# Performance work log

Measured on AMD Instinct MI355X. Metric: run time of the kernel, lower is better.

## Reference

```python
import jax, jax.numpy as jnp
import numpy as np


def gcn_conv(x, W, b, src, dst, num_nodes):
    # PyG GCNConv: h = D^{-1/2} (A + I) D^{-1/2} (x W) + b
    h = x @ W  # [N, H]
    ones = jnp.ones(src.shape[0], dtype=h.dtype)
    deg = jax.ops.segment_sum(ones, dst, num_segments=num_nodes) + 1.0  # +1 for self-loop
    d_inv_sqrt = jax.lax.rsqrt(deg)
    norm = d_inv_sqrt[src] * d_inv_sqrt[dst]  # [E]
    msg = h[src] * norm[:, None]  # [E, H] gather
    agg = jax.ops.segment_sum(msg, dst, num_segments=num_nodes)  # scatter-add
    agg = agg + h * (1.0 / deg)[:, None]  # self-loop term: deg_i^{-1/2} * deg_i^{-1/2}
    return agg + b


def setup_inputs() -> dict:
    key = jax.random.key(0)
    ks = jax.random.split(key, 10)
    N, E, F, H, C, G = 100000, 1000000, 64, 128, 2, 512
    x = jax.random.normal(ks[0], (N, F), dtype=jnp.float32)
    edge_index = jax.random.randint(ks[1], (2, E), 0, N, dtype=jnp.int64)
    batch = jnp.sort(jax.random.randint(ks[2], (N,), 0, G, dtype=jnp.int64))
    s1 = 1.0 / np.sqrt(F)
    s2 = 1.0 / np.sqrt(H)
    W1 = jax.random.normal(ks[3], (F, H), dtype=jnp.float32) * s1
    b1 = jnp.zeros((H,), dtype=jnp.float32)
    W2 = jax.random.normal(ks[4], (H, H), dtype=jnp.float32) * s2
    b2 = jnp.zeros((H,), dtype=jnp.float32)
    Wfc = jax.random.normal(ks[5], (H, C), dtype=jnp.float32) * s2
    bfc = jnp.zeros((C,), dtype=jnp.float32)
    return {"x": x, "edge_index": edge_index, "batch": batch, "num_graphs": G,
            "W1": W1, "b1": b1, "W2": W2, "b2": b2, "Wfc": Wfc, "bfc": bfc}


def reference(x, edge_index, batch, num_graphs, W1, b1, W2, b2, Wfc, bfc):
    # Dropout is inference-mode (identity), matching model.eval().
    N = x.shape[0]
    src, dst = edge_index[0], edge_index[1]
    h = gcn_conv(x, W1, b1, src, dst, N)
    h = jax.nn.relu(h)
    h = gcn_conv(h, W2, b2, src, dst, N)
    h = jax.nn.relu(h)
    # global mean pool over graphs
    summed = jax.ops.segment_sum(h, batch, num_segments=num_graphs)  # [G, H]
    counts = jax.ops.segment_sum(jnp.ones((N,), h.dtype), batch, num_segments=num_graphs)
    pooled = summed / jnp.maximum(counts, 1.0)[:, None]
    logits = pooled @ Wfc + bfc  # [G, C]
    return jax.nn.softmax(logits, axis=1)
```

## Files before the change

### kernel.cpp

```cpp
#include <hip/hip_runtime.h>
#include <hip/hip_bf16.h>

typedef __hip_bfloat16 bf16;
typedef __attribute__((ext_vector_type(8))) short short8;
typedef __attribute__((ext_vector_type(4))) float f32x4;
typedef __attribute__((ext_vector_type(2))) float f32x2;

#define FDIM 64
#define HDIM 128

#define ESTRIDE 4096
#define EC 8192
#define ECPT (EC / 256)

__device__ __forceinline__ float b2f(bf16 v) { return __bfloat162float(v); }
__device__ __forceinline__ float bits2f(unsigned int u) {
    return __uint_as_float(u << 16);
}
__device__ __forceinline__ unsigned short f2bits(float f) {
    bf16 b = __float2bfloat16(f);
    return *reinterpret_cast<unsigned short*>(&b);
}
__device__ __forceinline__ unsigned char f2fp8(float v) {
    int pk = __builtin_amdgcn_cvt_pk_fp8_f32(v, v, 0, false);
    return (unsigned char)(pk & 0xFF);
}

__device__ __forceinline__ int edge_word(const int* e, long long logical_idx, int is64) {
    return is64 ? e[2 * logical_idx] : e[logical_idx];
}

__global__ __launch_bounds__(256) void k_phase1(const int* __restrict__ edge,
                                                int* __restrict__ gcur,
                                                int* __restrict__ ebuf,
                                                int E,
                                                const void* __restrict__ W1, const void* __restrict__ b1,
                                                const void* __restrict__ W2, const void* __restrict__ b2,
                                                const void* __restrict__ Wfc, const void* __restrict__ bfc,
                                                bf16* __restrict__ W1t, bf16* __restrict__ W2t,
                                                bf16* __restrict__ b1c, bf16* __restrict__ b2c,
                                                bf16* __restrict__ Wfcc, bf16* __restrict__ bfcc,
                                                const void* __restrict__ x,
                                                unsigned char* __restrict__ X8,
                                                int totalX4,
                                                int* __restrict__ flags,
                                                const int* __restrict__ batch,
                                                int* __restrict__ gstart,
                                                int N, int G,
                                                int NB1, int WB, int XB) {
    int blk = blockIdx.x;
    int tid = threadIdx.x;
    if (blk < NB1) {
        unsigned long long zb = __ballot(edge[2 * (tid & 63) + 1] == 0);
        int is64 = (__popcll(zb) > 32);
        __shared__ int h[512];
        for (int b2 = tid; b2 < 512; b2 += 256) h[b2] = 0;
        __syncthreads();
        int e0 = blk * EC;
        int dcache[ECPT];
#pragma unroll
        for (int k = 0; k < ECPT; k++) {
            int i = e0 + (k << 8) + tid;
            int d = -1;
            if (i < E) d = edge_word(edge, (long long)E + i, is64);
            dcache[k] = d;
            if (d >= 0) atomicAdd(&h[(d >> 8) & 511], 1);
        }
        __syncthreads();
        for (int b2 = tid; b2 < 512; b2 += 256) {
            int c = h[b2];
            h[b2] = c ? atomicAdd(&gcur[b2], c) : 0;
        }
        __syncthreads();
#pragma unroll
        for (int k = 0; k < ECPT; k++) {
            int i = e0 + (k << 8) + tid;
            int d = dcache[k];
            if (d >= 0) {
                int s = edge_word(edge, i, is64);
                int bb = (d >> 8) & 511;
                int pos = atomicAdd(&h[bb], 1);
                if ((unsigned)pos < (unsigned)ESTRIDE)
                    ebuf[(bb << 12) + pos] = s | ((d & 255) << 24);
            }
        }
    } else if (blk < NB1 + WB) {
        const unsigned short* w1u = (const unsigned short*)W1;
        unsigned short wv = w1u[2 * (tid & 63)];
        int ee = (wv >> 7) & 0xFF;
        unsigned long long wb2 = __ballot(ee == 0 || ee >= 137);
        int f0 = (__popcll(wb2) > 4);
        if (blk == NB1 && tid == 0) flags[0] = f0;
        int gid = (blk - NB1) * 256 + tid;
        int stride = WB * 256;
#define CV(src, si) (f0 ? __float2bfloat16(((const float*)(src))[si]) : ((const bf16*)(src))[si])
        for (int i = gid; i < FDIM * HDIM; i += stride) {
            int n = i >> 6, k = i & 63;
            W1t[i] = CV(W1, k * HDIM + n);
        }
        for (int i = gid; i < HDIM * HDIM; i += stride) {
            int n = i >> 7, k = i & 127;
            W2t[i] = CV(W2, k * HDIM + n);
        }
        for (int i = gid; i < HDIM; i += stride) b1c[i] = CV(b1, i);
        for (int i = gid; i < HDIM; i += stride) b2c[i] = CV(b2, i);
        for (int i = gid; i < HDIM * 2; i += stride) Wfcc[i] = CV(Wfc, i);
        for (int i = gid; i < 2; i += stride) bfcc[i] = CV(bfc, i);
#undef CV
    } else if (blk < NB1 + WB + XB) {
        const unsigned short* w1u = (const unsigned short*)W1;
        unsigned short wv = w1u[2 * (tid & 63)];
        int ee = (wv >> 7) & 0xFF;
        unsigned long long wb2 = __ballot(ee == 0 || ee >= 137);
        int f0 = (__popcll(wb2) > 4);
        int t = (blk - NB1 - WB) * 256 + tid;
        if (t >= totalX4) return;
        float4 v;
        if (f0) {
            v = ((const float4*)x)[t];
        } else {
            uint2 p = ((const uint2*)x)[t];
            v.x = bits2f(p.x & 0xFFFFu); v.y = bits2f(p.x >> 16);
            v.z = bits2f(p.y & 0xFFFFu); v.w = bits2f(p.y >> 16);
        }
        unsigned int q0 = (unsigned int)__builtin_amdgcn_cvt_pk_fp8_f32(v.x, v.y, 0, false) & 0xFFFFu;
        unsigned int q1 = (unsigned int)__builtin_amdgcn_cvt_pk_fp8_f32(v.z, v.w, 0, false) & 0xFFFFu;
        ((unsigned int*)X8)[t] = (q1 << 16) | q0;
    } else {
        int bv = batch[1025 + 2 * (tid & 63)];
        unsigned long long bb2 = __ballot(bv == 0);
        int is64 = (__popcll(bb2) > 32);
        int i = (blk - NB1 - WB - XB) * 256 + tid;
        if (i >= N) return;
        int bi = is64 ? batch[2 * i] : batch[i];
        if (i == 0) {
            for (int g = 0; g <= bi; g++) gstart[g] = 0;
        } else {
            int bp = is64 ? batch[2 * (i - 1)] : batch[i - 1];
            for (int g = bp + 1; g <= bi; g++) gstart[g] = i;
        }
        if (i == N - 1) {
            for (int g = bi + 1; g <= G; g++) gstart[g] = N;
        }
    }
}

__global__ __launch_bounds__(256) void k_csr(const int* __restrict__ ebuf,
                                             const int* __restrict__ gcur,
                                             int* __restrict__ rowptr,
                                             int* __restrict__ cnt,
                                             float* __restrict__ dinv,
                                             int* __restrict__ srclist,
                                             int N) {
    __shared__ int sred[256];
    __shared__ int sc[256];
    __shared__ int sa[256], sb[256];
    int b = blockIdx.x;
    int tid = threadIdx.x;
    int part = 0;
    for (int j = tid; j < b; j += 256) {
        int v = gcur[j];
        part += (v > ESTRIDE) ? ESTRIDE : v;
    }
    sred[tid] = part;
    __syncthreads();
    for (int s = 128; s > 0; s >>= 1) {
        if (tid < s) sred[tid] += sred[tid + s];
        __syncthreads();
    }
    int gbase = sred[0];
    int cnt_b = gcur[b];
    if (cnt_b > ESTRIDE) cnt_b = ESTRIDE;
    sc[tid] = 0;
    __syncthreads();
    const int* eb = ebuf + (b << 12);
    for (int j = tid; j < cnt_b; j += 256) {
        int p = eb[j];
        atomicAdd(&sc[(unsigned)p >> 24], 1);
    }
    __syncthreads();
    int cval = sc[tid];
    sa[tid] = cval;
    __syncthreads();
    int* cur = sa; int* nxt = sb;
    for (int off = 1; off < 256; off <<= 1) {
        int v = cur[tid];
        if (tid >= off) v += cur[tid - off];
        nxt[tid] = v;
        __syncthreads();
        int* t = cur; cur = nxt; nxt = t;
    }
    int excl = cur[tid] - cval;
    int node = (b << 8) + tid;
    if (node < N) {
        rowptr[node] = gbase + excl;
        cnt[node] = cval;
        dinv[node] = rsqrtf((float)cval + 1.0f);
    }
    __syncthreads();
    sc[tid] = excl;
    __syncthreads();
    for (int j = tid; j < cnt_b; j += 256) {
        int p = eb[j];
        int pos = atomicAdd(&sc[(unsigned)p >> 24], 1);
        srclist[gbase + pos] = p & 0xFFFFFF;
    }
}

#define ACC8(u2, e) do { \
    f32x2 f01 = __builtin_amdgcn_cvt_pk_f32_fp8((u2).x, false); \
    f32x2 f23 = __builtin_amdgcn_cvt_pk_f32_fp8((u2).x, true); \
    f32x2 f45 = __builtin_amdgcn_cvt_pk_f32_fp8((u2).y, false); \
    f32x2 f67 = __builtin_amdgcn_cvt_pk_f32_fp8((u2).y, true); \
    acc[0] += f01[0] * (e); acc[1] += f01[1] * (e); \
    acc[2] += f23[0] * (e); acc[3] += f23[1] * (e); \
    acc[4] += f45[0] * (e); acc[5] += f45[1] * (e); \
    acc[6] += f67[0] * (e); acc[7] += f67[1] * (e); } while (0)

#define ACC4(w, e, o) do { \
    f32x2 fA = __builtin_amdgcn_cvt_pk_f32_fp8((w), false); \
    f32x2 fB = __builtin_amdgcn_cvt_pk_f32_fp8((w), true); \
    acc[(o)+0] += fA[0] * (e); acc[(o)+1] += fA[1] * (e); \
    acc[(o)+2] += fB[0] * (e); acc[(o)+3] += fB[1] * (e); } while (0)
#define ACC16(u4, e) do { ACC4((u4).x, (e), 0); ACC4((u4).y, (e), 4); \
                          ACC4((u4).z, (e), 8); ACC4((u4).w, (e), 12); } while (0)

__device__ __forceinline__ uint4 packbf16x8(const float* a) {
    uint4 p;
    p.x = ((unsigned int)f2bits(a[1]) << 16) | f2bits(a[0]);
    p.y = ((unsigned int)f2bits(a[3]) << 16) | f2bits(a[2]);
    p.z = ((unsigned int)f2bits(a[5]) << 16) | f2bits(a[4]);
    p.w = ((unsigned int)f2bits(a[7]) << 16) | f2bits(a[6]);
    return p;
}

#define LDCH(V, EV, c_, ROWW) do { \
    int jb_ = (c_) << 3; int mm_ = cnt - jb_; if (mm_ > 8) mm_ = 8; \
    int svl_ = srclist[start + jb_ + ((sub < mm_) ? sub : (mm_ - 1))]; \
    float dvl_ = dinv[svl_]; \
    _Pragma("unroll") \
    for (int t_ = 0; t_ < 8; t_++) { \
        int st_ = __shfl(svl_, lb + t_); float et_ = __shfl(dvl_, lb + t_); \
        EV[t_] = (t_ < mm_) ? et_ : 0.f; \
        V[t_] = hrow[(size_t)st_ * (ROWW) + sub]; \
    } } while (0)

__global__ __launch_bounds__(256) void k_agg64(const unsigned char* __restrict__ x8,
                                               const int* __restrict__ srclist,
                                               const int* __restrict__ rowptr,
                                               const int* __restrict__ count,
                                               const float* __restrict__ dinv,
                                               bf16* __restrict__ outb, int N) {
    int wave = threadIdx.x >> 6;
    int lane = threadIdx.x & 63;
    int group = lane >> 3;
    int sub = lane & 7;
    int i = blockIdx.x * 32 + wave * 8 + group;
    if (i >= N) return;
    int start = rowptr[i];
    int cnt = count[i];
    float di = dinv[i];
    const uint2* hrow = (const uint2*)x8;
    float acc[8] = {0.f, 0.f, 0.f, 0.f, 0.f, 0.f, 0.f, 0.f};
    int lb = group << 3;
    int nch = (cnt + 7) >> 3;
    uint2 vA[8], vB[8]; float eA[8], eB[8];
    if (nch == 2) {
        LDCH(vA, eA, 0, 8); LDCH(vB, eB, 1, 8);
#pragma unroll
        for (int t = 0; t < 8; t++) ACC8(vA[t], eA[t]);
#pragma unroll
        for (int t = 0; t < 8; t++) ACC8(vB[t], eB[t]);
    } else {
        for (int c = 0; c < nch; c++) {
            LDCH(vA, eA, c, 8);
#pragma unroll
            for (int t = 0; t < 8; t++) ACC8(vA[t], eA[t]);
        }
    }
    {
        uint2 vs = hrow[(size_t)i * 8 + sub];
        float self = di * di;
        float sacc[8] = {0.f, 0.f, 0.f, 0.f, 0.f, 0.f, 0.f, 0.f};
        {
            float* acc = sacc;
            ACC8(vs, self);
        }
#pragma unroll
        for (int k = 0; k < 8; k++) acc[k] = di * acc[k] + sacc[k];
    }
    uint4 pv = packbf16x8(acc);
    ((uint4*)outb)[(size_t)i * 8 + sub] = pv;
}

__global__ __launch_bounds__(256) void k_agg128(const unsigned char* __restrict__ h8,
                                                const int* __restrict__ srclist,
                                                const int* __restrict__ rowptr,
                                                const int* __restrict__ count,
                                                const float* __restrict__ dinv,
                                                bf16* __restrict__ outb, int N) {
    int wave = threadIdx.x >> 6;
    int lane = threadIdx.x & 63;
    int group = lane >> 3;
    int sub = lane & 7;
    int i = blockIdx.x * 32 + wave * 8 + group;
    if (i >= N) return;
    int start = rowptr[i];
    int cnt = count[i];
    float di = dinv[i];
    const uint4* hrow = (const uint4*)h8;
    float acc[16];
#pragma unroll
    for (int k = 0; k < 16; k++) acc[k] = 0.f;
    int lb = group << 3;
    int nch = (cnt + 7) >> 3;
    uint4 vA[8], vB[8]; float eA[8], eB[8];
    if (nch == 2) {
        LDCH(vA, eA, 0, 8); LDCH(vB, eB, 1, 8);
#pragma unroll
        for (int t = 0; t < 8; t++) ACC16(vA[t], eA[t]);
#pragma unroll
        for (int t = 0; t < 8; t++) ACC16(vB[t], eB[t]);
    } else {
        for (int c = 0; c < nch; c++) {
            LDCH(vA, eA, c, 8);
#pragma unroll
            for (int t = 0; t < 8; t++) ACC16(vA[t], eA[t]);
        }
    }
    {
        uint4 vs = hrow[(size_t)i * 8 + sub];
        float self = di * di;
        float sacc[16];
#pragma unroll
        for (int k = 0; k < 16; k++) sacc[k] = 0.f;
        {
            float* acc = sacc;
            ACC16(vs, self);
        }
#pragma unroll
        for (int k = 0; k < 16; k++) acc[k] = di * acc[k] + sacc[k];
    }
    uint4 p0 = packbf16x8(&acc[0]);
    uint4 p1 = packbf16x8(&acc[8]);
    ((uint4*)outb)[(size_t)i * 16 + sub * 2 + 0] = p0;
    ((uint4*)outb)[(size_t)i * 16 + sub * 2 + 1] = p1;
}

#define K1PAD 72
__global__ __launch_bounds__(256) void k_gemmA(const bf16* __restrict__ Y,
                                               const bf16* __restrict__ W1t,
                                               const bf16* __restrict__ bias,
                                               unsigned char* __restrict__ h8, int N) {
    __shared__ bf16 As[64 * K1PAD];
    __shared__ bf16 Wt[HDIM * K1PAD];
    __shared__ float bsf[HDIM];
    int tid = threadIdx.x;
    int base = blockIdx.x * 64;
    {
        const uint4* wsrc = (const uint4*)W1t;
        for (int i = tid; i < HDIM * 8; i += 256) {
            int n = i >> 3, c = i & 7;
            *(uint4*)&Wt[n * K1PAD + c * 8] = wsrc[n * 8 + c];
        }
    }
    {
        const uint4* xb = (const uint4*)Y;
        for (int i = tid; i < 64 * 8; i += 256) {
            int r = i >> 3, c = i & 7;
            int gr = base + r; if (gr >= N) gr = N - 1;
            *(uint4*)&As[r * K1PAD + c * 8] = xb[(size_t)gr * 8 + c];
        }
    }
    if (tid < HDIM) bsf[tid] = b2f(bias[tid]);
    __syncthreads();
    int wid = tid >> 6, lane = tid & 63;
    int l15 = lane & 15, q = lane >> 4;
    int m0 = wid * 16;
    short8 af[2];
#pragma unroll
    for (int kc = 0; kc < 2; kc++)
        af[kc] = *(const short8*)&As[(m0 + l15) * K1PAD + kc * 32 + q * 8];
    f32x4 acc[8];
#pragma unroll
    for (int nt = 0; nt < 8; nt++) {
        acc[nt] = (f32x4){0.f, 0.f, 0.f, 0.f};
#pragma unroll
        for (int kc = 0; kc < 2; kc++) {
            short8 bf = *(const short8*)&Wt[(nt * 16 + l15) * K1PAD + kc * 32 + q * 8];
            acc[nt] = __builtin_amdgcn_mfma_f32_16x16x32_bf16(af[kc], bf, acc[nt], 0, 0, 0);
        }
    }
#pragma unroll
    for (int nt = 0; nt < 8; nt++) {
        int col = nt * 16 + l15;
        float bv = bsf[col];
#pragma unroll
        for (int r = 0; r < 4; r++) {
            int gr = base + m0 + q * 4 + r;
            if (gr < N) {
                float v = fmaxf(acc[nt][r] + bv, 0.f);
                h8[(size_t)gr * HDIM + col] = f2fp8(v);
            }
        }
    }
}

#define K2PAD 136
__global__ __launch_bounds__(256) void k_gemmB(const bf16* __restrict__ Z,
                                               const bf16* __restrict__ W2t,
                                               const bf16* __restrict__ bias,
                                               bf16* __restrict__ outp, int N) {
    __shared__ bf16 As[64 * K2PAD];
    __shared__ bf16 Wt[HDIM * K2PAD];
    __shared__ float bsf[HDIM];
    int tid = threadIdx.x;
    int base = blockIdx.x * 64;
    {
        const uint4* wsrc = (const uint4*)W2t;
        for (int i = tid; i < HDIM * 16; i += 256) {
            int n = i >> 4, c = i & 15;
            *(uint4*)&Wt[n * K2PAD + c * 8] = wsrc[n * 16 + c];
        }
    }
    const uint4* xb = (const uint4*)Z;
    for (int i = tid; i < 64 * 16; i += 256) {
        int r = i >> 4, c = i & 15;
        int gr = base + r; if (gr >= N) gr = N - 1;
        *(uint4*)&As[r * K2PAD + c * 8] = xb[(size_t)gr * 16 + c];
    }
    if (tid < HDIM) bsf[tid] = b2f(bias[tid]);
    __syncthreads();
    int wid = tid >> 6, lane = tid & 63;
    int l15 = lane & 15, q = lane >> 4;
    int m0 = wid * 16;
    short8 af[4];
#pragma unroll
    for (int kc = 0; kc < 4; kc++)
        af[kc] = *(const short8*)&As[(m0 + l15) * K2PAD + kc * 32 + q * 8];
    f32x4 acc[8];
#pragma unroll
    for (int nt = 0; nt < 8; nt++) {
        acc[nt] = (f32x4){0.f, 0.f, 0.f, 0.f};
#pragma unroll
        for (int kc = 0; kc < 4; kc++) {
            short8 bf = *(const short8*)&Wt[(nt * 16 + l15) * K2PAD + kc * 32 + q * 8];
            acc[nt] = __builtin_amdgcn_mfma_f32_16x16x32_bf16(af[kc], bf, acc[nt], 0, 0, 0);
        }
    }
#pragma unroll
    for (int nt = 0; nt < 8; nt++) {
        int col = nt * 16 + l15;
        float bv = bsf[col];
#pragma unroll
        for (int r = 0; r < 4; r++) {
            int gr = base + m0 + q * 4 + r;
            if (gr < N) outp[(size_t)gr * HDIM + col] = __float2bfloat16(fmaxf(acc[nt][r] + bv, 0.f));
        }
    }
}

__global__ __launch_bounds__(256) void k_pool(const bf16* __restrict__ hact,
                                              const int* __restrict__ gstart,
                                              const bf16* __restrict__ Wfc,
                                              const bf16* __restrict__ bfc,
                                              void* __restrict__ out,
                                              const int* __restrict__ flags) {
    __shared__ float lds[16][HDIM + 1];
    __shared__ float colsum[HDIM];
    int g = blockIdx.x;
    int s = gstart[g], e = gstart[g + 1];
    int tid = threadIdx.x;
    int cslot = tid & 15;
    int rslot = tid >> 4;
    const uint4* hp = (const uint4*)hact;
    float a[8] = {0.f, 0.f, 0.f, 0.f, 0.f, 0.f, 0.f, 0.f};
    for (int r = s + rslot; r < e; r += 16) {
        uint4 v = hp[(size_t)r * 16 + cslot];
        a[0] += bits2f(v.x & 0xFFFFu); a[1] += bits2f(v.x >> 16);
        a[2] += bits2f(v.y & 0xFFFFu); a[3] += bits2f(v.y >> 16);
        a[4] += bits2f(v.z & 0xFFFFu); a[5] += bits2f(v.z >> 16);
        a[6] += bits2f(v.w & 0xFFFFu); a[7] += bits2f(v.w >> 16);
    }
#pragma unroll
    for (int k = 0; k < 8; k++) lds[rslot][cslot * 8 + k] = a[k];
    __syncthreads();
    if (tid < HDIM) {
        float sum = 0.f;
#pragma unroll
        for (int k = 0; k < 16; k++) sum += lds[k][tid];
        colsum[tid] = sum;
    }
    __syncthreads();
    if (tid >= 64) return;
    int lane = tid;
    float inv = 1.0f / fmaxf((float)(e - s), 1.0f);
    float m0 = colsum[2 * lane] * inv;
    float m1 = colsum[2 * lane + 1] * inv;
    float l0 = m0 * b2f(Wfc[(2 * lane) * 2 + 0]) + m1 * b2f(Wfc[(2 * lane + 1) * 2 + 0]);
    float l1 = m0 * b2f(Wfc[(2 * lane) * 2 + 1]) + m1 * b2f(Wfc[(2 * lane + 1) * 2 + 1]);
    for (int sft = 32; sft; sft >>= 1) { l0 += __shfl_down(l0, sft); l1 += __shfl_down(l1, sft); }
    if (lane == 0) {
        float z0 = l0 + b2f(bfc[0]);
        float z1 = l1 + b2f(bfc[1]);
        float mx = fmaxf(z0, z1);
        float e0 = expf(z0 - mx), e1 = expf(z1 - mx);
        float sm = e0 + e1;
        float p0 = e0 / sm, p1 = e1 / sm;
        if (flags[0]) {
            ((float*)out)[2 * g + 0] = p0;
            ((float*)out)[2 * g + 1] = p1;
        } else {
            ((bf16*)out)[2 * g + 0] = __float2bfloat16(p0);
            ((bf16*)out)[2 * g + 1] = __float2bfloat16(p1);
        }
    }
}

extern "C" void kernel_launch(void* const* d_in, const int* in_sizes, int n_in,
                              void* d_out, int out_size, void* d_ws, size_t ws_size,
                              hipStream_t stream) {
    const void* x    = d_in[0];
    const int*  edge = (const int*)d_in[1];
    const int*  batch= (const int*)d_in[2];
    const void* W1  = d_in[4];
    const void* b1  = d_in[5];
    const void* W2  = d_in[6];
    const void* b2  = d_in[7];
    const void* Wfc = d_in[8];
    const void* bfc = d_in[9];

    int N = in_sizes[0] / FDIM;
    int E = in_sizes[1] / 2;
    int G = out_size / 2;

    int*   flags  = (int*)d_ws;
    float* dinv   = (float*)((char*)d_ws + 64);
    int*   gcur   = (int*)(dinv + N);
    int*   gstart = gcur + 512;
    int*   rowptr = gstart + 516;
    int*   count  = rowptr + N;
    int*   srclist= count + N;
    int*   ebuf   = srclist + E;
    bf16*  Abuf   = (bf16*)(ebuf + 512 * ESTRIDE);
    bf16*  Bbuf   = Abuf + (size_t)N * HDIM;
    bf16*  b1c    = Bbuf + (size_t)N * HDIM;
    bf16*  b2c    = b1c + HDIM;
    bf16*  Wfcc   = b2c + HDIM;
    bf16*  bfcc   = Wfcc + 256;
    bf16*  W1t    = bfcc + 64;
    bf16*  W2t    = W1t + FDIM * HDIM;
    unsigned char* H8 = (unsigned char*)(W2t + HDIM * HDIM);
    unsigned char* X8 = H8 + (size_t)N * HDIM;

    bf16* Y = Abuf;
    bf16* Z = Abuf;

    int NB  = (N + 255) >> 8;
    int NB1 = (E + EC - 1) / EC;
    int WB = 32;
    int XB = (N * 16 + 255) / 256;
    int BB = (N + 255) / 256;
    int totalX4 = N * 16;

    hipMemsetAsync(gcur, 0, 512 * sizeof(int), stream);
    k_phase1<<<NB1 + WB + XB + BB, 256, 0, stream>>>(edge, gcur, ebuf, E,
                                                     W1, b1, W2, b2, Wfc, bfc,
                                                     W1t, W2t, b1c, b2c, Wfcc, bfcc,
                                                     x, X8, totalX4, flags,
                                                     batch, gstart, N, G,
                                                     NB1, WB, XB);
    k_csr<<<NB, 256, 0, stream>>>(ebuf, gcur, rowptr, count, dinv, srclist, N);

    k_agg64<<<(N + 31) / 32, 256, 0, stream>>>(X8, srclist, rowptr, count, dinv, Y, N);
    k_gemmA<<<(N + 63) / 64, 256, 0, stream>>>(Y, W1t, b1c, H8, N);

    k_agg128<<<(N + 31) / 32, 256, 0, stream>>>(H8, srclist, rowptr, count, dinv, Z, N);
    k_gemmB<<<(N + 63) / 64, 256, 0, stream>>>(Z, W2t, b2c, Bbuf, N);

    k_pool<<<G, 256, 0, stream>>>(Bbuf, gstart, Wfcc, bfcc, d_out, flags);
}
```

Baseline: 225.9 us.

## Store features as column-slice planes so each thread aggregates one node per slice

```diff
diff --git a/kernel.cpp b/kernel.cpp
--- a/kernel.cpp
+++ b/kernel.cpp
@@ -125,7 +125,8 @@
         }
         unsigned int q0 = (unsigned int)__builtin_amdgcn_cvt_pk_fp8_f32(v.x, v.y, 0, false) & 0xFFFFu;
         unsigned int q1 = (unsigned int)__builtin_amdgcn_cvt_pk_fp8_f32(v.z, v.w, 0, false) & 0xFFFFu;
-        ((unsigned int*)X8)[t] = (q1 << 16) | q0;
+        int node = t >> 4, sl = (t >> 1) & 7, w = t & 1;
+        ((unsigned int*)X8)[((size_t)sl * N + node) * 2 + w] = (q1 << 16) | q0;
     } else {
         int bv = batch[1025 + 2 * (tid & 63)];
         unsigned long long bb2 = __ballot(bv == 0);
@@ -234,52 +235,34 @@
     return p;
 }
 
-#define LDCH(V, EV, c_, ROWW) do { \
-    int jb_ = (c_) << 3; int mm_ = cnt - jb_; if (mm_ > 8) mm_ = 8; \
-    int svl_ = srclist[start + jb_ + ((sub < mm_) ? sub : (mm_ - 1))]; \
-    float dvl_ = dinv[svl_]; \
-    _Pragma("unroll") \
-    for (int t_ = 0; t_ < 8; t_++) { \
-        int st_ = __shfl(svl_, lb + t_); float et_ = __shfl(dvl_, lb + t_); \
-        EV[t_] = (t_ < mm_) ? et_ : 0.f; \
-        V[t_] = hrow[(size_t)st_ * (ROWW) + sub]; \
-    } } while (0)
-
-__global__ __launch_bounds__(256) void k_agg64(const unsigned char* __restrict__ x8,
+__global__ __launch_bounds__(256) void k_agg64(const unsigned char* __restrict__ x8s,
                                                const int* __restrict__ srclist,
                                                const int* __restrict__ rowptr,
                                                const int* __restrict__ count,
                                                const float* __restrict__ dinv,
-                                               bf16* __restrict__ outb, int N) {
-    int wave = threadIdx.x >> 6;
-    int lane = threadIdx.x & 63;
-    int group = lane >> 3;
-    int sub = lane & 7;
-    int i = blockIdx.x * 32 + wave * 8 + group;
-    if (i >= N) return;
-    int start = rowptr[i];
-    int cnt = count[i];
-    float di = dinv[i];
-    const uint2* hrow = (const uint2*)x8;
+                                               uint4* __restrict__ ys, int N) {
+    int slice = blockIdx.x & 7;
+    int node = (blockIdx.x >> 3) * 256 + threadIdx.x;
+    if (node >= N) return;
+    const uint2* plane = (const uint2*)(x8s + (size_t)slice * N * 8);
+    int start = rowptr[node];
+    int cnt = count[node];
+    float di = dinv[node];
     float acc[8] = {0.f, 0.f, 0.f, 0.f, 0.f, 0.f, 0.f, 0.f};
-    int lb = group << 3;
-    int nch = (cnt + 7) >> 3;
-    uint2 vA[8], vB[8]; float eA[8], eB[8];
-    if (nch == 2) {
-        LDCH(vA, eA, 0, 8); LDCH(vB, eB, 1, 8);
-#pragma unroll
-        for (int t = 0; t < 8; t++) ACC8(vA[t], eA[t]);
-#pragma unroll
-        for (int t = 0; t < 8; t++) ACC8(vB[t], eB[t]);
-    } else {
-        for (int c = 0; c < nch; c++) {
-            LDCH(vA, eA, c, 8);
-#pragma unroll
-            for (int t = 0; t < 8; t++) ACC8(vA[t], eA[t]);
-        }
+    for (int j = 0; j < cnt; j += 8) {
+        int m = cnt - j; if (m > 8) m = 8;
+        int idx[8]; uint2 v[8]; float w[8];
+#pragma unroll
+        for (int t = 0; t < 8; t++) idx[t] = srclist[start + j + ((t < m) ? t : (m - 1))];
+#pragma unroll
+        for (int t = 0; t < 8; t++) v[t] = plane[idx[t]];
+#pragma unroll
+        for (int t = 0; t < 8; t++) w[t] = (t < m) ? dinv[idx[t]] : 0.f;
+#pragma unroll
+        for (int t = 0; t < 8; t++) ACC8(v[t], w[t]);
     }
     {
-        uint2 vs = hrow[(size_t)i * 8 + sub];
+        uint2 vs = plane[node];
         float self = di * di;
         float sacc[8] = {0.f, 0.f, 0.f, 0.f, 0.f, 0.f, 0.f, 0.f};
         {
@@ -289,47 +272,39 @@
 #pragma unroll
         for (int k = 0; k < 8; k++) acc[k] = di * acc[k] + sacc[k];
     }
-    uint4 pv = packbf16x8(acc);
-    ((uint4*)outb)[(size_t)i * 8 + sub] = pv;
-}
-
-__global__ __launch_bounds__(256) void k_agg128(const unsigned char* __restrict__ h8,
+    ys[(size_t)slice * N + node] = packbf16x8(acc);
+}
+
+__global__ __launch_bounds__(256) void k_agg128(const unsigned char* __restrict__ h8s,
                                                 const int* __restrict__ srclist,
                                                 const int* __restrict__ rowptr,
                                                 const int* __restrict__ count,
                                                 const float* __restrict__ dinv,
-                                                bf16* __restrict__ outb, int N) {
-    int wave = threadIdx.x >> 6;
-    int lane = threadIdx.x & 63;
-    int group = lane >> 3;
-    int sub = lane & 7;
-    int i = blockIdx.x * 32 + wave * 8 + group;
-    if (i >= N) return;
-    int start = rowptr[i];
-    int cnt = count[i];
-    float di = dinv[i];
-    const uint4* hrow = (const uint4*)h8;
+                                                uint4* __restrict__ zs, int N) {
+    int slice = blockIdx.x & 7;
+    int node = (blockIdx.x >> 3) * 256 + threadIdx.x;
+    if (node >= N) return;
+    const uint4* plane = (const uint4*)(h8s + (size_t)slice * N * 16);
+    int start = rowptr[node];
+    int cnt = count[node];
+    float di = dinv[node];
     float acc[16];
 #pragma unroll
     for (int k = 0; k < 16; k++) acc[k] = 0.f;
-    int lb = group << 3;
-    int nch = (cnt + 7) >> 3;
-    uint4 vA[8], vB[8]; float eA[8], eB[8];
-    if (nch == 2) {
-        LDCH(vA, eA, 0, 8); LDCH(vB, eB, 1, 8);
-#pragma unroll
-        for (int t = 0; t < 8; t++) ACC16(vA[t], eA[t]);
-#pragma unroll
-        for (int t = 0; t < 8; t++) ACC16(vB[t], eB[t]);
-    } else {
-        for (int c = 0; c < nch; c++) {
-            LDCH(vA, eA, c, 8);
-#pragma unroll
-            for (int t = 0; t < 8; t++) ACC16(vA[t], eA[t]);
-        }
+    for (int j = 0; j < cnt; j += 8) {
+        int m = cnt - j; if (m > 8) m = 8;
+        int idx[8]; uint4 v[8]; float w[8];
+#pragma unroll
+        for (int t = 0; t < 8; t++) idx[t] = srclist[start + j + ((t < m) ? t : (m - 1))];
+#pragma unroll
+        for (int t = 0; t < 8; t++) v[t] = plane[idx[t]];
+#pragma unroll
+        for (int t = 0; t < 8; t++) w[t] = (t < m) ? dinv[idx[t]] : 0.f;
+#pragma unroll
+        for (int t = 0; t < 8; t++) ACC16(v[t], w[t]);
     }
     {
-        uint4 vs = hrow[(size_t)i * 8 + sub];
+        uint4 vs = plane[node];
         float self = di * di;
         float sacc[16];
 #pragma unroll
@@ -343,15 +318,15 @@
     }
     uint4 p0 = packbf16x8(&acc[0]);
     uint4 p1 = packbf16x8(&acc[8]);
-    ((uint4*)outb)[(size_t)i * 16 + sub * 2 + 0] = p0;
-    ((uint4*)outb)[(size_t)i * 16 + sub * 2 + 1] = p1;
+    zs[((size_t)slice * N + node) * 2 + 0] = p0;
+    zs[((size_t)slice * N + node) * 2 + 1] = p1;
 }
 
 #define K1PAD 72
 __global__ __launch_bounds__(256) void k_gemmA(const bf16* __restrict__ Y,
                                                const bf16* __restrict__ W1t,
                                                const bf16* __restrict__ bias,
-                                               unsigned char* __restrict__ h8, int N) {
+                                               unsigned char* __restrict__ h8s, int N) {
     __shared__ bf16 As[64 * K1PAD];
     __shared__ bf16 Wt[HDIM * K1PAD];
     __shared__ float bsf[HDIM];
@@ -365,11 +340,11 @@
         }
     }
     {
-        const uint4* xb = (const uint4*)Y;
+        const uint4* yb = (const uint4*)Y;
         for (int i = tid; i < 64 * 8; i += 256) {
-            int r = i >> 3, c = i & 7;
+            int c = i >> 6, r = i & 63;
             int gr = base + r; if (gr >= N) gr = N - 1;
-            *(uint4*)&As[r * K1PAD + c * 8] = xb[(size_t)gr * 8 + c];
+            *(uint4*)&As[r * K1PAD + c * 8] = yb[(size_t)c * N + gr];
         }
     }
     if (tid < HDIM) bsf[tid] = b2f(bias[tid]);
@@ -393,14 +368,13 @@
     }
 #pragma unroll
     for (int nt = 0; nt < 8; nt++) {
-        int col = nt * 16 + l15;
-        float bv = bsf[col];
+        float bv = bsf[nt * 16 + l15];
 #pragma unroll
         for (int r = 0; r < 4; r++) {
             int gr = base + m0 + q * 4 + r;
             if (gr < N) {
                 float v = fmaxf(acc[nt][r] + bv, 0.f);
-                h8[(size_t)gr * HDIM + col] = f2fp8(v);
+                h8s[(size_t)nt * N * 16 + (size_t)gr * 16 + l15] = f2fp8(v);
             }
         }
     }
@@ -423,11 +397,16 @@
             *(uint4*)&Wt[n * K2PAD + c * 8] = wsrc[n * 16 + c];
         }
     }
-    const uint4* xb = (const uint4*)Z;
-    for (int i = tid; i < 64 * 16; i += 256) {
-        int r = i >> 4, c = i & 15;
-        int gr = base + r; if (gr >= N) gr = N - 1;
-        *(uint4*)&As[r * K2PAD + c * 8] = xb[(size_t)gr * 16 + c];
+    {
+        const uint4* zb = (const uint4*)Z;
+        for (int i = tid; i < 64 * 8; i += 256) {
+            int s3 = i >> 6, r = i & 63;
+            int gr = base + r; if (gr >= N) gr = N - 1;
+            uint4 a0 = zb[((size_t)s3 * N + gr) * 2 + 0];
+            uint4 a1 = zb[((size_t)s3 * N + gr) * 2 + 1];
+            *(uint4*)&As[r * K2PAD + s3 * 16 + 0] = a0;
+            *(uint4*)&As[r * K2PAD + s3 * 16 + 8] = a1;
+        }
     }
     if (tid < HDIM) bsf[tid] = b2f(bias[tid]);
     __syncthreads();
@@ -562,6 +541,7 @@
     int XB = (N * 16 + 255) / 256;
     int BB = (N + 255) / 256;
     int totalX4 = N * 16;
+    int NBn = (N + 255) / 256;
 
     hipMemsetAsync(gcur, 0, 512 * sizeof(int), stream);
     k_phase1<<<NB1 + WB + XB + BB, 256, 0, stream>>>(edge, gcur, ebuf, E,
@@ -572,10 +552,10 @@
                                                      NB1, WB, XB);
     k_csr<<<NB, 256, 0, stream>>>(ebuf, gcur, rowptr, count, dinv, srclist, N);
 
-    k_agg64<<<(N + 31) / 32, 256, 0, stream>>>(X8, srclist, rowptr, count, dinv, Y, N);
+    k_agg64<<<NBn * 8, 256, 0, stream>>>(X8, srclist, rowptr, count, dinv, (uint4*)Y, N);
     k_gemmA<<<(N + 63) / 64, 256, 0, stream>>>(Y, W1t, b1c, H8, N);
 
-    k_agg128<<<(N + 31) / 32, 256, 0, stream>>>(H8, srclist, rowptr, count, dinv, Z, N);
+    k_agg128<<<NBn * 8, 256, 0, stream>>>(H8, srclist, rowptr, count, dinv, (uint4*)Z, N);
     k_gemmB<<<(N + 63) / 64, 256, 0, stream>>>(Z, W2t, b2c, Bbuf, N);
 
     k_pool<<<G, 256, 0, stream>>>(Bbuf, gstart, Wfcc, bfcc, d_out, flags);
```

Result: slower. 310.8 us (+37.6%).

## Split layer-2 features into column slices for cache-local aggregation

Applied to the files above, without the earlier changes.

```diff
diff --git a/kernel.cpp b/kernel.cpp
--- a/kernel.cpp
+++ b/kernel.cpp
@@ -293,43 +293,37 @@
     ((uint4*)outb)[(size_t)i * 8 + sub] = pv;
 }
 
-__global__ __launch_bounds__(256) void k_agg128(const unsigned char* __restrict__ h8,
+__global__ __launch_bounds__(256) void k_agg128(const unsigned char* __restrict__ h8s,
                                                 const int* __restrict__ srclist,
                                                 const int* __restrict__ rowptr,
                                                 const int* __restrict__ count,
                                                 const float* __restrict__ dinv,
-                                                bf16* __restrict__ outb, int N) {
-    int wave = threadIdx.x >> 6;
-    int lane = threadIdx.x & 63;
-    int group = lane >> 3;
-    int sub = lane & 7;
-    int i = blockIdx.x * 32 + wave * 8 + group;
-    if (i >= N) return;
-    int start = rowptr[i];
-    int cnt = count[i];
-    float di = dinv[i];
-    const uint4* hrow = (const uint4*)h8;
+                                                uint4* __restrict__ zs, int N) {
+    int slice = blockIdx.x & 3;
+    int node = (blockIdx.x >> 2) * 128 + (threadIdx.x >> 1);
+    int sub = threadIdx.x & 1;
+    if (node >= N) return;
+    const uint4* plane = (const uint4*)(h8s + (size_t)slice * N * 32);
+    int start = rowptr[node];
+    int cnt = count[node];
+    float di = dinv[node];
     float acc[16];
 #pragma unroll
     for (int k = 0; k < 16; k++) acc[k] = 0.f;
-    int lb = group << 3;
-    int nch = (cnt + 7) >> 3;
-    uint4 vA[8], vB[8]; float eA[8], eB[8];
-    if (nch == 2) {
-        LDCH(vA, eA, 0, 8); LDCH(vB, eB, 1, 8);
-#pragma unroll
-        for (int t = 0; t < 8; t++) ACC16(vA[t], eA[t]);
-#pragma unroll
-        for (int t = 0; t < 8; t++) ACC16(vB[t], eB[t]);
-    } else {
-        for (int c = 0; c < nch; c++) {
-            LDCH(vA, eA, c, 8);
-#pragma unroll
-            for (int t = 0; t < 8; t++) ACC16(vA[t], eA[t]);
-        }
+    for (int j = 0; j < cnt; j += 8) {
+        int m = cnt - j; if (m > 8) m = 8;
+        int idx[8]; uint4 v[8]; float w[8];
+#pragma unroll
+        for (int t = 0; t < 8; t++) idx[t] = srclist[start + j + ((t < m) ? t : (m - 1))];
+#pragma unroll
+        for (int t = 0; t < 8; t++) v[t] = plane[(size_t)idx[t] * 2 + sub];
+#pragma unroll
+        for (int t = 0; t < 8; t++) w[t] = (t < m) ? dinv[idx[t]] : 0.f;
+#pragma unroll
+        for (int t = 0; t < 8; t++) ACC16(v[t], w[t]);
     }
     {
-        uint4 vs = hrow[(size_t)i * 8 + sub];
+        uint4 vs = plane[(size_t)node * 2 + sub];
         float self = di * di;
         float sacc[16];
 #pragma unroll
@@ -343,15 +337,16 @@
     }
     uint4 p0 = packbf16x8(&acc[0]);
     uint4 p1 = packbf16x8(&acc[8]);
-    ((uint4*)outb)[(size_t)i * 16 + sub * 2 + 0] = p0;
-    ((uint4*)outb)[(size_t)i * 16 + sub * 2 + 1] = p1;
+    size_t zo = (size_t)slice * N * 4 + (size_t)node * 4 + sub * 2;
+    zs[zo + 0] = p0;
+    zs[zo + 1] = p1;
 }
 
 #define K1PAD 72
 __global__ __launch_bounds__(256) void k_gemmA(const bf16* __restrict__ Y,
                                                const bf16* __restrict__ W1t,
                                                const bf16* __restrict__ bias,
-                                               unsigned char* __restrict__ h8, int N) {
+                                               unsigned char* __restrict__ h8s, int N) {
     __shared__ bf16 As[64 * K1PAD];
     __shared__ bf16 Wt[HDIM * K1PAD];
     __shared__ float bsf[HDIM];
@@ -395,12 +390,13 @@
     for (int nt = 0; nt < 8; nt++) {
         int col = nt * 16 + l15;
         float bv = bsf[col];
+        int sl = col >> 5, cb = col & 31;
 #pragma unroll
         for (int r = 0; r < 4; r++) {
             int gr = base + m0 + q * 4 + r;
             if (gr < N) {
                 float v = fmaxf(acc[nt][r] + bv, 0.f);
-                h8[(size_t)gr * HDIM + col] = f2fp8(v);
+                h8s[(size_t)sl * N * 32 + (size_t)gr * 32 + cb] = f2fp8(v);
             }
         }
     }
@@ -423,11 +419,16 @@
             *(uint4*)&Wt[n * K2PAD + c * 8] = wsrc[n * 16 + c];
         }
     }
-    const uint4* xb = (const uint4*)Z;
-    for (int i = tid; i < 64 * 16; i += 256) {
-        int r = i >> 4, c = i & 15;
+    {
+        const uint4* zb = (const uint4*)Z;
+        int s3 = tid >> 6, r = tid & 63;
         int gr = base + r; if (gr >= N) gr = N - 1;
-        *(uint4*)&As[r * K2PAD + c * 8] = xb[(size_t)gr * 16 + c];
+        const uint4* src = &zb[(size_t)s3 * N * 4 + (size_t)gr * 4];
+        uint4 a0 = src[0], a1 = src[1], a2 = src[2], a3 = src[3];
+        *(uint4*)&As[r * K2PAD + s3 * 32 + 0]  = a0;
+        *(uint4*)&As[r * K2PAD + s3 * 32 + 8]  = a1;
+        *(uint4*)&As[r * K2PAD + s3 * 32 + 16] = a2;
+        *(uint4*)&As[r * K2PAD + s3 * 32 + 24] = a3;
     }
     if (tid < HDIM) bsf[tid] = b2f(bias[tid]);
     __syncthreads();
@@ -575,7 +576,8 @@
     k_agg64<<<(N + 31) / 32, 256, 0, stream>>>(X8, srclist, rowptr, count, dinv, Y, N);
     k_gemmA<<<(N + 63) / 64, 256, 0, stream>>>(Y, W1t, b1c, H8, N);
 
-    k_agg128<<<(N + 31) / 32, 256, 0, stream>>>(H8, srclist, rowptr, count, dinv, Z, N);
+    k_agg128<<<((N + 127) / 128) * 4, 256, 0, stream>>>(H8, srclist, rowptr, count, dinv,
+                                                        (uint4*)Z, N);
     k_gemmB<<<(N + 63) / 64, 256, 0, stream>>>(Z, W2t, b2c, Bbuf, N);
 
     k_pool<<<G, 256, 0, stream>>>(Bbuf, gstart, Wfcc, bfcc, d_out, flags);
```

Result: slower. 238.0 us (+5.3%).

## Stage edge bucketing in shared memory and rewrite gather loop with exact-count chunks

Applied to the files above, without the earlier changes.

```diff
diff --git a/kernel.cpp b/kernel.cpp
--- a/kernel.cpp
+++ b/kernel.cpp
@@ -10,7 +10,7 @@
 #define HDIM 128
 
 #define ESTRIDE 4096
-#define EC 8192
+#define EC 4096
 #define ECPT (EC / 256)
 
 __device__ __forceinline__ float b2f(bf16 v) { return __bfloat162float(v); }
@@ -48,12 +48,17 @@
                                                 int* __restrict__ gstart,
                                                 int N, int G,
                                                 int NB1, int WB, int XB) {
+    __shared__ int h[512];
+    __shared__ int lb2[512];
+    __shared__ int gb[512];
+    __shared__ int stage[EC];
+    __shared__ unsigned short aux[EC];
+    __shared__ int s1[256], s2[256];
     int blk = blockIdx.x;
     int tid = threadIdx.x;
     if (blk < NB1) {
         unsigned long long zb = __ballot(edge[2 * (tid & 63) + 1] == 0);
         int is64 = (__popcll(zb) > 32);
-        __shared__ int h[512];
         for (int b2 = tid; b2 < 512; b2 += 256) h[b2] = 0;
         __syncthreads();
         int e0 = blk * EC;
@@ -67,10 +72,24 @@
             if (d >= 0) atomicAdd(&h[(d >> 8) & 511], 1);
         }
         __syncthreads();
-        for (int b2 = tid; b2 < 512; b2 += 256) {
-            int c = h[b2];
-            h[b2] = c ? atomicAdd(&gcur[b2], c) : 0;
-        }
+        int a0 = h[2 * tid], a1 = h[2 * tid + 1];
+        s1[tid] = a0 + a1;
+        __syncthreads();
+        int* cur = s1; int* nxt = s2;
+        for (int off = 1; off < 256; off <<= 1) {
+            int v = cur[tid];
+            if (tid >= off) v += cur[tid - off];
+            nxt[tid] = v;
+            __syncthreads();
+            int* t = cur; cur = nxt; nxt = t;
+        }
+        int excl = cur[tid] - (a0 + a1);
+        lb2[2 * tid] = excl;
+        lb2[2 * tid + 1] = excl + a0;
+        gb[2 * tid]     = a0 ? atomicAdd(&gcur[2 * tid], a0) : 0;
+        gb[2 * tid + 1] = a1 ? atomicAdd(&gcur[2 * tid + 1], a1) : 0;
+        h[2 * tid] = lb2[2 * tid];
+        h[2 * tid + 1] = lb2[2 * tid + 1];
         __syncthreads();
 #pragma unroll
         for (int k = 0; k < ECPT; k++) {
@@ -80,9 +99,17 @@
                 int s = edge_word(edge, i, is64);
                 int bb = (d >> 8) & 511;
                 int pos = atomicAdd(&h[bb], 1);
-                if ((unsigned)pos < (unsigned)ESTRIDE)
-                    ebuf[(bb << 12) + pos] = s | ((d & 255) << 24);
+                stage[pos] = s | ((d & 255) << 24);
+                aux[pos] = (unsigned short)bb;
             }
+        }
+        __syncthreads();
+        int total = (e0 + EC <= E) ? EC : (E - e0);
+        for (int j = tid; j < total; j += 256) {
+            int bb = aux[j];
+            int tgt = gb[bb] + (j - lb2[bb]);
+            if ((unsigned)tgt < (unsigned)ESTRIDE)
+                ebuf[(bb << 12) + tgt] = stage[j];
         }
     } else if (blk < NB1 + WB) {
         const unsigned short* w1u = (const unsigned short*)W1;
@@ -313,19 +340,36 @@
 #pragma unroll
     for (int k = 0; k < 16; k++) acc[k] = 0.f;
     int lb = group << 3;
-    int nch = (cnt + 7) >> 3;
-    uint4 vA[8], vB[8]; float eA[8], eB[8];
-    if (nch == 2) {
-        LDCH(vA, eA, 0, 8); LDCH(vB, eB, 1, 8);
-#pragma unroll
-        for (int t = 0; t < 8; t++) ACC16(vA[t], eA[t]);
-#pragma unroll
-        for (int t = 0; t < 8; t++) ACC16(vB[t], eB[t]);
-    } else {
-        for (int c = 0; c < nch; c++) {
-            LDCH(vA, eA, c, 8);
-#pragma unroll
-            for (int t = 0; t < 8; t++) ACC16(vA[t], eA[t]);
+    for (int jb = 0; jb < cnt; jb += 8) {
+        int m = cnt - jb; if (m > 8) m = 8;
+        int sv = srclist[start + jb + ((sub < m) ? sub : (m - 1))];
+        float dvv = dinv[sv];
+        if (m == 8) {
+            int s[8]; float e[8]; uint4 v[8];
+#pragma unroll
+            for (int t = 0; t < 8; t++) { s[t] = __shfl(sv, lb + t); e[t] = __shfl(dvv, lb + t); }
+#pragma unroll
+            for (int t = 0; t < 8; t++) v[t] = hrow[(size_t)s[t] * 8 + sub];
+#pragma unroll
+            for (int t = 0; t < 8; t++) ACC16(v[t], e[t]);
+        } else {
+            int j = 0;
+            for (; j + 4 <= m; j += 4) {
+                int s0 = __shfl(sv, lb + j + 0); float e0 = __shfl(dvv, lb + j + 0);
+                int s1 = __shfl(sv, lb + j + 1); float e1 = __shfl(dvv, lb + j + 1);
+                int s2 = __shfl(sv, lb + j + 2); float e2 = __shfl(dvv, lb + j + 2);
+                int s3 = __shfl(sv, lb + j + 3); float e3 = __shfl(dvv, lb + j + 3);
+                uint4 v0 = hrow[(size_t)s0 * 8 + sub];
+                uint4 v1 = hrow[(size_t)s1 * 8 + sub];
+                uint4 v2 = hrow[(size_t)s2 * 8 + sub];
+                uint4 v3 = hrow[(size_t)s3 * 8 + sub];
+                ACC16(v0, e0); ACC16(v1, e1); ACC16(v2, e2); ACC16(v3, e3);
+            }
+            for (; j < m; j++) {
+                int s0 = __shfl(sv, lb + j); float e0 = __shfl(dvv, lb + j);
+                uint4 v0 = hrow[(size_t)s0 * 8 + sub];
+                ACC16(v0, e0);
+            }
         }
     }
     {
```

After: 222.9 us. About the same (-1.3%).
